# Performance work log

Measured on AMD Instinct MI355X. Metric: run time of the kernel, lower is better.

Reference implementation:

```python
import jax, jax.numpy as jnp
import numpy as np
from jax import lax

B, S, T = 4096, 4096, 2  # batch, seq_length, num_tags (CRF(2) hardcoded in ToNySegmenter)


def setup_inputs() -> dict:
    key = jax.random.key(0)
    k_em, k_st, k_en, k_tr, k_tg, k_len = jax.random.split(key, 6)
    emissions = jax.random.normal(k_em, (B, S, T), dtype=jnp.float32)
    start_transitions = jax.random.uniform(k_st, (T,), dtype=jnp.float32, minval=-1.0, maxval=1.0)
    end_transitions = jax.random.uniform(k_en, (T,), dtype=jnp.float32, minval=-1.0, maxval=1.0)
    transitions = jax.random.uniform(k_tr, (T, T), dtype=jnp.float32, minval=-1.0, maxval=1.0)
    tags = jax.random.randint(k_tg, (B, S), 0, T, dtype=jnp.int64)
    # variable-length sequences; first position always valid (CRF assumes mask[0]==1)
    lengths = jax.random.randint(k_len, (B,), S // 2, S + 1)
    mask = (jnp.arange(S)[None, :] < lengths[:, None]).astype(jnp.int32)
    return {
        'emissions': emissions,
        'start_transitions': start_transitions,
        'end_transitions': end_transitions,
        'transitions': transitions,
        'tags': tags,
        'mask': mask,
    }


def _crf_nll(emissions, start_transitions, end_transitions, transitions, tags, mask):
    # batch_first=True in the torch module -> transpose to time-major (S, B, ...)
    em = jnp.transpose(emissions, (1, 0, 2))      # (S, B, T)
    tg = tags.T                                   # (S, B)
    mk = mask.T.astype(em.dtype)                  # (S, B)
    seq_len, batch = tg.shape

    # ---- numerator: score of the gold path (fully vectorized over time) ----
    emit = jnp.take_along_axis(em, tg[..., None], axis=2)[..., 0]   # (S, B)
    score = start_transitions[tg[0]] + emit[0]                      # (B,)
    trans = transitions[tg[:-1], tg[1:]]                            # (S-1, B)
    score = score + jnp.sum((trans + emit[1:]) * mk[1:], axis=0)
    seq_ends = mk.sum(axis=0).astype(jnp.int32) - 1                 # (B,)
    last_tags = tg[seq_ends, jnp.arange(batch)]
    score = score + end_transitions[last_tags]

    # ---- denominator: forward algorithm via lax.scan over time ----
    init = start_transitions + em[0]                                # (B, T)

    def step(s, x):
        e_i, m_i = x                                                # (B,T), (B,)
        # s[b, prev] + transitions[prev, cur] + e_i[b, cur], logsumexp over prev
        ns = jax.nn.logsumexp(s[:, :, None] + transitions[None, :, :] + e_i[:, None, :], axis=1)
        s = jnp.where(m_i[:, None] > 0, ns, s)
        return s, None

    final, _ = lax.scan(step, init, (em[1:], mk[1:]))
    normalizer = jax.nn.logsumexp(final + end_transitions, axis=1)  # (B,)

    return -(score - normalizer).mean()


def reference(emissions, start_transitions, end_transitions, transitions, tags, mask):
    return _crf_nll(emissions, start_transitions, end_transitions, transitions, tags, mask)
```

## Files before the change

### kernel.cpp

```cpp
#include <hip/hip_runtime.h>

#define B_CONST 4096
#define S_CONST 4096

#define NEGBIG (-1e30f)

__device__ __forceinline__ float lse2(float a, float b) {
    float m = fmaxf(a, b);
    float d = fminf(a, b) - m;
    return m + __logf(1.0f + __expf(d));
}

struct Seg { float m00, m01, m10, m11; };

__device__ __forceinline__ Seg seg_compose(const Seg& L, const Seg& R) {
    Seg o;
    o.m00 = lse2(L.m00 + R.m00, L.m01 + R.m10);
    o.m01 = lse2(L.m00 + R.m01, L.m01 + R.m11);
    o.m10 = lse2(L.m10 + R.m00, L.m11 + R.m10);
    o.m11 = lse2(L.m10 + R.m01, L.m11 + R.m11);
    return o;
}

__global__ __launch_bounds__(256) void crf_row_kernel(
    const float* __restrict__ em,
    const float* __restrict__ st,
    const float* __restrict__ en,
    const float* __restrict__ tr,
    const int*   __restrict__ tags,
    const int*   __restrict__ mask,
    float* __restrict__ out)
{
    const int b    = blockIdx.x;
    const int tid  = threadIdx.x;
    const int lane = tid & 63;
    const int wid  = tid >> 6;
    const int cb   = wid << 10;
    const int c0   = cb + (lane << 4);

    const float* em_row = em   + (size_t)b * S_CONST * 2;
    const int*   tg_row = tags + (size_t)b * S_CONST;
    const int*   mk     = mask + (size_t)b * S_CONST;

    int v1 = mk[lane << 6];
    unsigned long long bal1 = __ballot(v1 != 0);
    int base = (__popcll(bal1) - 1) << 6;
    int v2 = mk[base + lane];
    const int L = base + __popcll(__ballot(v2 != 0));

    const float t00 = tr[0], t01 = tr[1], t10 = tr[2], t11 = tr[3];

    Seg seg; seg.m00 = 0.0f; seg.m11 = 0.0f; seg.m01 = NEGBIG; seg.m10 = NEGBIG;
    float sc = 0.0f;

    __shared__ float4 wseg[4];
    __shared__ float  wsc[4];

    if (cb < L) {
        const int4* tv = (const int4*)(tg_row + c0);
        int4 tq0 = tv[0], tq1 = tv[1], tq2 = tv[2], tq3 = tv[3];
        const float4* ev = (const float4*)(em_row + 2 * c0);
        float4 e0 = ev[0], e1 = ev[1], e2 = ev[2], e3 = ev[3];
        float4 e4 = ev[4], e5 = ev[5], e6 = ev[6], e7 = ev[7];

        int prev = __shfl_up(tq3.w, 1);
        if (lane == 0) prev = (cb > 0) ? tg_row[cb - 1] : 0;

        const int myHi = min(c0 + 16, L);
        const int lo   = (c0 == 0) ? 1 : c0;

        #define STEP(T_, E0_, E1_, TG_)                                      \
            do {                                                             \
                int t_ = (T_);                                               \
                if (t_ >= 1 && t_ < myHi) {                                  \
                    float e0_ = (E0_), e1_ = (E1_);                          \
                    Seg M;                                                   \
                    M.m00 = t00 + e0_; M.m01 = t01 + e1_;                    \
                    M.m10 = t10 + e0_; M.m11 = t11 + e1_;                    \
                    if (t_ == lo) seg = M;                                   \
                    else          seg = seg_compose(seg, M);                 \
                    float trv = prev ? ((TG_) ? t11 : t10)                   \
                                     : ((TG_) ? t01 : t00);                  \
                    sc += trv + ((TG_) ? e1_ : e0_);                         \
                }                                                            \
                prev = (TG_);                                                \
            } while (0)

        STEP(c0 +  0, e0.x, e0.y, tq0.x);
        STEP(c0 +  1, e0.z, e0.w, tq0.y);
        STEP(c0 +  2, e1.x, e1.y, tq0.z);
        STEP(c0 +  3, e1.z, e1.w, tq0.w);
        STEP(c0 +  4, e2.x, e2.y, tq1.x);
        STEP(c0 +  5, e2.z, e2.w, tq1.y);
        STEP(c0 +  6, e3.x, e3.y, tq1.z);
        STEP(c0 +  7, e3.z, e3.w, tq1.w);
        STEP(c0 +  8, e4.x, e4.y, tq2.x);
        STEP(c0 +  9, e4.z, e4.w, tq2.y);
        STEP(c0 + 10, e5.x, e5.y, tq2.z);
        STEP(c0 + 11, e5.z, e5.w, tq2.w);
        STEP(c0 + 12, e6.x, e6.y, tq3.x);
        STEP(c0 + 13, e6.z, e6.w, tq3.y);
        STEP(c0 + 14, e7.x, e7.y, tq3.z);
        STEP(c0 + 15, e7.z, e7.w, tq3.w);
        #undef STEP

        #pragma unroll
        for (int s = 1; s < 64; s <<= 1) {
            Seg r;
            r.m00 = __shfl_down(seg.m00, s);
            r.m01 = __shfl_down(seg.m01, s);
            r.m10 = __shfl_down(seg.m10, s);
            r.m11 = __shfl_down(seg.m11, s);
            float rsc = __shfl_down(sc, s);
            seg = seg_compose(seg, r);
            sc += rsc;
        }
    }

    if (lane == 0) {
        wseg[wid] = make_float4(seg.m00, seg.m01, seg.m10, seg.m11);
        wsc[wid]  = sc;
    }
    __syncthreads();

    if (tid == 0) {
        float4 v = wseg[0];
        Seg P; P.m00 = v.x; P.m01 = v.y; P.m10 = v.z; P.m11 = v.w;
        float scT = wsc[0];
        #pragma unroll
        for (int w = 1; w < 4; ++w) {
            float4 rv = wseg[w];
            Seg R; R.m00 = rv.x; R.m01 = rv.y; R.m10 = rv.z; R.m11 = rv.w;
            P = seg_compose(P, R);
            scT += wsc[w];
        }

        float e00 = em_row[0], e01 = em_row[1];
        float st0 = st[0], st1 = st[1];
        float en0 = en[0], en1 = en[1];

        float i0 = st0 + e00, i1 = st1 + e01;
        float f0 = lse2(i0 + P.m00, i1 + P.m10);
        float f1 = lse2(i0 + P.m01, i1 + P.m11);
        float norm = lse2(f0 + en0, f1 + en1);

        int tg0 = tg_row[0];
        int tgL = tg_row[L - 1];
        float score = (tg0 ? st1 : st0) + (tg0 ? e01 : e00) + scT
                    + (tgL ? en1 : en0);

        atomicAdd(out, (norm - score) * (1.0f / (float)B_CONST));
    }
}

extern "C" void kernel_launch(void* const* d_in, const int* in_sizes, int n_in,
                              void* d_out, int out_size, void* d_ws, size_t ws_size,
                              hipStream_t stream) {
    const float* em   = (const float*)d_in[0];
    const float* st   = (const float*)d_in[1];
    const float* en   = (const float*)d_in[2];
    const float* tr   = (const float*)d_in[3];
    const int*   tags = (const int*)d_in[4];
    const int*   mask = (const int*)d_in[5];

    float* out = (float*)d_out;

    hipMemsetAsync(out, 0, sizeof(float) * out_size, stream);
    crf_row_kernel<<<B_CONST, 256, 0, stream>>>(em, st, en, tr, tags, mask, out);
}
```

Before: 286.1 us.

## Replace log-space CRF segment composition with linear-space products and exponent renormalization

Switches the forward-algorithm segment matrices from log-semiring (logsumexp per entry) to linear-space 2x2 matrix products, with frexp/ldexp renormalization that tracks a separate integer exponent. This removes the exp/log transcendentals inside every compose, leaving only one exp2 per emission value. It also specializes the fully-valid chunk case so per-step bounds checks drop out. The cost is a change in numerical behaviour, with a risk of underflow or precision loss between renormalizations, and the wave-level reductions now also run for fully masked threads.

```diff
diff --git a/kernel.cpp b/kernel.cpp
--- a/kernel.cpp
+++ b/kernel.cpp
@@ -1,24 +1,34 @@
 #include <hip/hip_runtime.h>
+#include <type_traits>
 
 #define B_CONST 4096
 #define S_CONST 4096
 
-#define NEGBIG (-1e30f)
+#define LOG2E 1.44269504088896340736f
+#define LN2   0.69314718055994530942f
 
-__device__ __forceinline__ float lse2(float a, float b) {
-    float m = fmaxf(a, b);
-    float d = fminf(a, b) - m;
-    return m + __logf(1.0f + __expf(d));
+struct Lin { float p00, p01, p10, p11, sc; int s; };
+
+__device__ __forceinline__ void lin_renorm(Lin& P) {
+    float m = fmaxf(fmaxf(P.p00, P.p01), fmaxf(P.p10, P.p11));
+    int ex;
+    (void)frexpf(m, &ex);
+    P.p00 = ldexpf(P.p00, -ex);
+    P.p01 = ldexpf(P.p01, -ex);
+    P.p10 = ldexpf(P.p10, -ex);
+    P.p11 = ldexpf(P.p11, -ex);
+    P.s += ex;
 }
 
-struct Seg { float m00, m01, m10, m11; };
-
-__device__ __forceinline__ Seg seg_compose(const Seg& L, const Seg& R) {
-    Seg o;
-    o.m00 = lse2(L.m00 + R.m00, L.m01 + R.m10);
-    o.m01 = lse2(L.m00 + R.m01, L.m01 + R.m11);
-    o.m10 = lse2(L.m10 + R.m00, L.m11 + R.m10);
-    o.m11 = lse2(L.m10 + R.m01, L.m11 + R.m11);
+__device__ __forceinline__ Lin lin_compose(const Lin& A, const Lin& B) {
+    Lin o;
+    o.p00 = A.p00 * B.p00 + A.p01 * B.p10;
+    o.p01 = A.p00 * B.p01 + A.p01 * B.p11;
+    o.p10 = A.p10 * B.p00 + A.p11 * B.p10;
+    o.p11 = A.p10 * B.p01 + A.p11 * B.p11;
+    o.s   = A.s + B.s;
+    o.sc  = A.sc + B.sc;
+    lin_renorm(o);
     return o;
 }
 
@@ -49,14 +59,13 @@
     const int L = base + __popcll(__ballot(v2 != 0));
 
     const float t00 = tr[0], t01 = tr[1], t10 = tr[2], t11 = tr[3];
+    const float l00 = exp2f(t00 * LOG2E), l01 = exp2f(t01 * LOG2E);
+    const float l10 = exp2f(t10 * LOG2E), l11 = exp2f(t11 * LOG2E);
 
-    Seg seg; seg.m00 = 0.0f; seg.m11 = 0.0f; seg.m01 = NEGBIG; seg.m10 = NEGBIG;
-    float sc = 0.0f;
+    Lin P; P.p00 = 1.0f; P.p01 = 0.0f; P.p10 = 0.0f; P.p11 = 1.0f;
+    P.s = 0; P.sc = 0.0f;
 
-    __shared__ float4 wseg[4];
-    __shared__ float  wsc[4];
-
-    if (cb < L) {
+    if (c0 < L) {
         const int4* tv = (const int4*)(tg_row + c0);
         int4 tq0 = tv[0], tq1 = tv[1], tq2 = tv[2], tq3 = tv[3];
         const float4* ev = (const float4*)(em_row + 2 * c0);
@@ -66,87 +75,93 @@
         int prev = __shfl_up(tq3.w, 1);
         if (lane == 0) prev = (cb > 0) ? tg_row[cb - 1] : 0;
 
-        const int myHi = min(c0 + 16, L);
-        const int lo   = (c0 == 0) ? 1 : c0;
+        const bool isz = (c0 == 0);
+        const float u00 = isz ? 1.0f : l00, u01 = isz ? 0.0f : l01;
+        const float u10 = isz ? 0.0f : l10, u11 = isz ? 1.0f : l11;
+        const float fg0 = isz ? 0.0f : 1.0f;
 
-        #define STEP(T_, E0_, E1_, TG_)                                      \
-            do {                                                             \
-                int t_ = (T_);                                               \
-                if (t_ >= 1 && t_ < myHi) {                                  \
-                    float e0_ = (E0_), e1_ = (E1_);                          \
-                    Seg M;                                                   \
-                    M.m00 = t00 + e0_; M.m01 = t01 + e1_;                    \
-                    M.m10 = t10 + e0_; M.m11 = t11 + e1_;                    \
-                    if (t_ == lo) seg = M;                                   \
-                    else          seg = seg_compose(seg, M);                 \
-                    float trv = prev ? ((TG_) ? t11 : t10)                   \
-                                     : ((TG_) ? t01 : t00);                  \
-                    sc += trv + ((TG_) ? e1_ : e0_);                         \
-                }                                                            \
-                prev = (TG_);                                                \
-            } while (0)
+        float sc = 0.0f;
 
-        STEP(c0 +  0, e0.x, e0.y, tq0.x);
-        STEP(c0 +  1, e0.z, e0.w, tq0.y);
-        STEP(c0 +  2, e1.x, e1.y, tq0.z);
-        STEP(c0 +  3, e1.z, e1.w, tq0.w);
-        STEP(c0 +  4, e2.x, e2.y, tq1.x);
-        STEP(c0 +  5, e2.z, e2.w, tq1.y);
-        STEP(c0 +  6, e3.x, e3.y, tq1.z);
-        STEP(c0 +  7, e3.z, e3.w, tq1.w);
-        STEP(c0 +  8, e4.x, e4.y, tq2.x);
-        STEP(c0 +  9, e4.z, e4.w, tq2.y);
-        STEP(c0 + 10, e5.x, e5.y, tq2.z);
-        STEP(c0 + 11, e5.z, e5.w, tq2.w);
-        STEP(c0 + 12, e6.x, e6.y, tq3.x);
-        STEP(c0 + 13, e6.z, e6.w, tq3.y);
-        STEP(c0 + 14, e7.x, e7.y, tq3.z);
-        STEP(c0 + 15, e7.z, e7.w, tq3.w);
-        #undef STEP
+        auto body = [&](auto FC) {
+            constexpr bool F = decltype(FC)::value;
+            #define DSTEP(G_, E0_, E1_, TG_, U00_, U01_, U10_, U11_, FG_)          \
+                do {                                                               \
+                    if (F || (c0 + (G_) < L)) {                                    \
+                        float d0 = exp2f((E0_) * LOG2E);                           \
+                        float d1 = exp2f((E1_) * LOG2E);                           \
+                        float a_ = P.p00 * (U00_) + P.p01 * (U10_);                \
+                        float b_ = P.p00 * (U01_) + P.p01 * (U11_);                \
+                        float c_ = P.p10 * (U00_) + P.p11 * (U10_);                \
+                        float d_ = P.p10 * (U01_) + P.p11 * (U11_);                \
+                        P.p00 = a_ * d0; P.p01 = b_ * d1;                          \
+                        P.p10 = c_ * d0; P.p11 = d_ * d1;                          \
+                        float trv = prev ? ((TG_) ? t11 : t10)                     \
+                                         : ((TG_) ? t01 : t00);                    \
+                        sc += (FG_) * (trv + ((TG_) ? (E1_) : (E0_)));             \
+                    }                                                              \
+                    prev = (TG_);                                                  \
+                } while (0)
 
-        #pragma unroll
-        for (int s = 1; s < 64; s <<= 1) {
-            Seg r;
-            r.m00 = __shfl_down(seg.m00, s);
-            r.m01 = __shfl_down(seg.m01, s);
-            r.m10 = __shfl_down(seg.m10, s);
-            r.m11 = __shfl_down(seg.m11, s);
-            float rsc = __shfl_down(sc, s);
-            seg = seg_compose(seg, r);
-            sc += rsc;
-        }
+            DSTEP( 0, e0.x, e0.y, tq0.x, u00, u01, u10, u11, fg0);
+            DSTEP( 1, e0.z, e0.w, tq0.y, l00, l01, l10, l11, 1.0f);
+            DSTEP( 2, e1.x, e1.y, tq0.z, l00, l01, l10, l11, 1.0f);
+            DSTEP( 3, e1.z, e1.w, tq0.w, l00, l01, l10, l11, 1.0f);
+            DSTEP( 4, e2.x, e2.y, tq1.x, l00, l01, l10, l11, 1.0f);
+            DSTEP( 5, e2.z, e2.w, tq1.y, l00, l01, l10, l11, 1.0f);
+            DSTEP( 6, e3.x, e3.y, tq1.z, l00, l01, l10, l11, 1.0f);
+            DSTEP( 7, e3.z, e3.w, tq1.w, l00, l01, l10, l11, 1.0f);
+            lin_renorm(P);
+            DSTEP( 8, e4.x, e4.y, tq2.x, l00, l01, l10, l11, 1.0f);
+            DSTEP( 9, e4.z, e4.w, tq2.y, l00, l01, l10, l11, 1.0f);
+            DSTEP(10, e5.x, e5.y, tq2.z, l00, l01, l10, l11, 1.0f);
+            DSTEP(11, e5.z, e5.w, tq2.w, l00, l01, l10, l11, 1.0f);
+            DSTEP(12, e6.x, e6.y, tq3.x, l00, l01, l10, l11, 1.0f);
+            DSTEP(13, e6.z, e6.w, tq3.y, l00, l01, l10, l11, 1.0f);
+            DSTEP(14, e7.x, e7.y, tq3.z, l00, l01, l10, l11, 1.0f);
+            DSTEP(15, e7.z, e7.w, tq3.w, l00, l01, l10, l11, 1.0f);
+            #undef DSTEP
+        };
+        if (c0 + 16 <= L) body(std::true_type{});
+        else              body(std::false_type{});
+
+        lin_renorm(P);
+        P.sc = sc;
     }
 
-    if (lane == 0) {
-        wseg[wid] = make_float4(seg.m00, seg.m01, seg.m10, seg.m11);
-        wsc[wid]  = sc;
+    #pragma unroll
+    for (int sft = 1; sft < 64; sft <<= 1) {
+        Lin R;
+        R.p00 = __shfl_down(P.p00, sft);
+        R.p01 = __shfl_down(P.p01, sft);
+        R.p10 = __shfl_down(P.p10, sft);
+        R.p11 = __shfl_down(P.p11, sft);
+        R.sc  = __shfl_down(P.sc,  sft);
+        R.s   = __shfl_down(P.s,   sft);
+        P = lin_compose(P, R);
     }
+
+    __shared__ Lin wseg[4];
+    if (lane == 0) wseg[wid] = P;
     __syncthreads();
 
     if (tid == 0) {
-        float4 v = wseg[0];
-        Seg P; P.m00 = v.x; P.m01 = v.y; P.m10 = v.z; P.m11 = v.w;
-        float scT = wsc[0];
+        Lin T4 = wseg[0];
         #pragma unroll
-        for (int w = 1; w < 4; ++w) {
-            float4 rv = wseg[w];
-            Seg R; R.m00 = rv.x; R.m01 = rv.y; R.m10 = rv.z; R.m11 = rv.w;
-            P = seg_compose(P, R);
-            scT += wsc[w];
-        }
+        for (int w = 1; w < 4; ++w) T4 = lin_compose(T4, wseg[w]);
 
         float e00 = em_row[0], e01 = em_row[1];
         float st0 = st[0], st1 = st[1];
         float en0 = en[0], en1 = en[1];
 
-        float i0 = st0 + e00, i1 = st1 + e01;
-        float f0 = lse2(i0 + P.m00, i1 + P.m10);
-        float f1 = lse2(i0 + P.m01, i1 + P.m11);
-        float norm = lse2(f0 + en0, f1 + en1);
+        float uu0 = exp2f(st0 * LOG2E), uu1 = exp2f(st1 * LOG2E);
+        float f0 = uu0 * T4.p00 + uu1 * T4.p10;
+        float f1 = uu0 * T4.p01 + uu1 * T4.p11;
+        float z  = f0 * exp2f(en0 * LOG2E) + f1 * exp2f(en1 * LOG2E);
+        float norm = (log2f(z) + (float)T4.s) * LN2;
 
         int tg0 = tg_row[0];
         int tgL = tg_row[L - 1];
-        float score = (tg0 ? st1 : st0) + (tg0 ? e01 : e00) + scT
+        float score = (tg0 ? st1 : st0) + (tg0 ? e01 : e00) + T4.sc
                     + (tgL ? en1 : en0);
 
         atomicAdd(out, (norm - score) * (1.0f / (float)B_CONST));
```

After: 444.3 us. 55.3% more time.
